# Kernel optimization log

Hardware: AMD Instinct MI355X
Metric: run time of the kernel (lower is better)

The kernel has to match this reference:

```python
import jax, jax.numpy as jnp
import numpy as np

B, TV, TS, DIN, D = 32, 1024, 64, 1024, 512
EPS = 1e-15


def setup_inputs() -> dict:
    key = jax.random.key(0)
    k1, k2, k3, k4, k5, k6 = jax.random.split(key, 6)
    videos = jax.random.normal(k1, (B, TV, DIN), dtype=jnp.float32)
    sentences = jax.random.normal(k2, (B, TS, DIN), dtype=jnp.float32)
    lengths = jax.random.randint(k3, (B,), 1, TS, dtype=jnp.int32)
    scale = 1.0 / np.sqrt(DIN)
    Wv = jax.random.normal(k4, (DIN, D), dtype=jnp.float32) * scale
    bv = jnp.zeros((D,), dtype=jnp.float32)
    Ws = jax.random.normal(k5, (DIN, D), dtype=jnp.float32) * scale
    bs = jnp.zeros((D,), dtype=jnp.float32)
    return {"videos": videos, "sentences": sentences, "lengths": lengths,
            "Wv": Wv, "bv": bv, "Ws": Ws, "bs": bs}


def _pair_score(V, S):
    # V: [TV, D] video repr for item i; S: [TS, D] sentence repr for item j
    nv = jnp.linalg.norm(V, axis=1)                      # [TV]
    ns = jnp.linalg.norm(S, axis=1)                      # [TS]
    # cosine-similarity coattention matrix via normalized matmul (no repeat/tile)
    C = (V @ S.T) / (nv[:, None] * ns[None, :] + EPS)    # [TV, TS]
    A = jax.nn.softmax(C, axis=1)                        # normalize over sentence axis
    att = A @ S                                          # [TV, D] sentence attention
    num = jnp.sum(V * att, axis=1)                       # [TV]
    den = nv * jnp.linalg.norm(att, axis=1)
    score = num / (den + EPS)                            # [TV] per-frame video score
    return jax.nn.logsumexp(score)                       # scalar


def reference(videos, sentences, lengths, Wv, bv, Ws, bs):
    # per-timestep dense encoders (video_layer / sentence_layer)
    videos_repr = jnp.einsum('btf,fd->btd', videos, Wv) + bv      # [B, TV, D]
    sentences_repr = jnp.einsum('bsf,fd->bsd', sentences, Ws) + bs  # [B, TS, D]
    # all-pairs (i video, j sentence) scores, vectorized over the B x B grid
    pairwise = jax.vmap(lambda V: jax.vmap(lambda S: _pair_score(V, S))(sentences_repr))
    scores_videos = pairwise(videos_repr)                # [B, B]
    return scores_videos
```

## Files before the change

### kernel.cpp

```cpp
#include <hip/hip_runtime.h>
#include <hip/hip_bf16.h>
#include <stdint.h>
#include <math.h>

typedef __attribute__((ext_vector_type(8))) __bf16 bf16x8;
typedef __attribute__((ext_vector_type(4))) float f32x4;

#define B_   32
#define TV_  1024
#define TS_  64
#define DIN_ 1024
#define D_   512

static __device__ __forceinline__ unsigned short f2bf(float f) {
    union { float f; uint32_t u; } x; x.f = f;
    uint32_t r = x.u + 0x7fffu + ((x.u >> 16) & 1u);
    return (unsigned short)(r >> 16);
}
static __device__ __forceinline__ uint32_t cvtpk(float lo, float hi) {
    uint32_t r;
    asm("v_cvt_pk_bf16_f32 %0, %1, %2" : "=v"(r) : "v"(lo), "v"(hi));
    return r;
}
static __device__ __forceinline__ void swap32(uint32_t& a, uint32_t& b) {
    asm volatile("v_permlane32_swap_b32 %0, %1" : "+v"(a), "+v"(b));
}
static __device__ __forceinline__ void swap16(uint32_t& a, uint32_t& b) {
    asm volatile("v_permlane16_swap_b32 %0, %1" : "+v"(a), "+v"(b));
}
static __device__ __forceinline__ void gload16(const void* g, void* l) {
    __builtin_amdgcn_global_load_lds((const __attribute__((address_space(1))) uint32_t*)g,
                                     (__attribute__((address_space(3))) uint32_t*)l, 16, 0, 0);
}

__global__ __launch_bounds__(256) void transpose_w(const float* __restrict__ Wv,
                                                   const float* __restrict__ Wsn,
                                                   unsigned short* __restrict__ Wt) {
    const int w = blockIdx.z;
    const float* src = w ? Wsn : Wv;
    __shared__ float t[32][33];
    const int k0 = blockIdx.x * 32, n0 = blockIdx.y * 32;
    const int tx = threadIdx.x & 31, ty = threadIdx.x >> 5;
    #pragma unroll
    for (int r = 0; r < 32; r += 8)
        t[r + ty][tx] = src[(size_t)(k0 + r + ty) * D_ + n0 + tx];
    __syncthreads();
    #pragma unroll
    for (int r = 0; r < 32; r += 8)
        Wt[(size_t)w * 524288 + (size_t)(n0 + r + ty) * DIN_ + k0 + tx] = f2bf(t[tx][r + ty]);
}

__global__ __launch_bounds__(256) void encoder_gemm(const float* __restrict__ videos,
                                                    const float* __restrict__ sentences,
                                                    const unsigned short* __restrict__ Wt,
                                                    const float* __restrict__ bv,
                                                    const float* __restrict__ bs,
                                                    unsigned short* __restrict__ Vrep,
                                                    unsigned short* __restrict__ Srep) {
    __shared__ char Asb[128 * 128];
    __shared__ char Bsb[128 * 128];
    const int bid = blockIdx.x;
    const float* X; const unsigned short* W; const float* bias; unsigned short* out;
    int m0, n0;
    if (bid < 1024) {
        int xcd = bid & 7, sl = bid >> 3;
        m0 = (xcd * 32 + (sl >> 2)) * 128;
        n0 = (sl & 3) * 128;
        X = videos; W = Wt; bias = bv; out = Vrep;
    } else {
        int sb = bid - 1024;
        m0 = (sb >> 2) * 128;
        n0 = (sb & 3) * 128;
        X = sentences; W = Wt + 524288; bias = bs; out = Srep;
    }
    const int tid = threadIdx.x;
    const int lane = tid & 63, wid = tid >> 6;
    const int g = lane >> 4, c = lane & 15;
    const int wm = wid >> 1, wn = wid & 1;

    f32x4 acc[4][4];
    {
        f32x4 z = {0.f, 0.f, 0.f, 0.f};
        #pragma unroll
        for (int a = 0; a < 4; ++a)
            #pragma unroll
            for (int b = 0; b < 4; ++b) acc[a][b] = z;
    }

    for (int kk = 0; kk < 16; ++kk) {
        const int k0 = kk * 64;
        #pragma unroll
        for (int it = 0; it < 8; ++it) {
            int idx = it * 256 + tid;
            int m = idx >> 4, k4 = idx & 15;
            float4 v = *(const float4*)(X + (size_t)(m0 + m) * DIN_ + k0 + k4 * 4);
            uint2 pk;
            pk.x = cvtpk(v.x, v.y);
            pk.y = cvtpk(v.z, v.w);
            *(uint2*)(Asb + m * 128 + ((k4 * 8) ^ ((m & 7) << 4))) = pk;
        }
        #pragma unroll
        for (int t = 0; t < 4; ++t) {
            int row = wid * 32 + t * 8 + (lane >> 3);
            const unsigned short* src = W + (size_t)(n0 + row) * DIN_ + k0 + (lane & 7) * 8;
            gload16(src, Bsb + wid * 4096 + t * 1024);
        }
        __syncthreads();
        #pragma unroll
        for (int ks = 0; ks < 2; ++ks) {
            bf16x8 a[4], b[4];
            #pragma unroll
            for (int mt = 0; mt < 4; ++mt) {
                int row = wm * 64 + mt * 16 + c;
                a[mt] = *(const bf16x8*)(Asb + row * 128 + ((g * 16 + ks * 64) ^ ((c & 7) << 4)));
            }
            #pragma unroll
            for (int nt = 0; nt < 4; ++nt) {
                int rowb = wn * 64 + nt * 16 + c;
                b[nt] = *(const bf16x8*)(Bsb + rowb * 128 + (g * 16 + ks * 64));
            }
            #pragma unroll
            for (int mt = 0; mt < 4; ++mt)
                #pragma unroll
                for (int nt = 0; nt < 4; ++nt)
                    acc[mt][nt] = __builtin_amdgcn_mfma_f32_16x16x32_bf16(a[mt], b[nt], acc[mt][nt], 0, 0, 0);
        }
        __syncthreads();
    }
    #pragma unroll
    for (int nt = 0; nt < 4; ++nt) {
        int col = n0 + wn * 64 + nt * 16 + c;
        float bb = bias[col];
        #pragma unroll
        for (int mt = 0; mt < 4; ++mt) {
            int rbase = m0 + wm * 64 + mt * 16 + g * 4;
            #pragma unroll
            for (int r = 0; r < 4; ++r)
                out[(size_t)(rbase + r) * D_ + col] = f2bf(acc[mt][nt][r] + bb);
        }
    }
}

__global__ __launch_bounds__(256) void rownorm_kernel(const unsigned short* __restrict__ R,
                                                      float* __restrict__ nrm, int nrows) {
    const int row = blockIdx.x * 4 + (threadIdx.x >> 6);
    const int lane = threadIdx.x & 63;
    if (row >= nrows) return;
    uint4 v = ((const uint4*)(R + (size_t)row * D_))[lane];
    float s = 0.f;
    uint32_t wsx[4] = {v.x, v.y, v.z, v.w};
    #pragma unroll
    for (int q = 0; q < 4; ++q) {
        float lo = __uint_as_float(wsx[q] << 16);
        float hi = __uint_as_float(wsx[q] & 0xffff0000u);
        s += lo * lo + hi * hi;
    }
    #pragma unroll
    for (int d = 1; d < 64; d <<= 1) s += __shfl_xor(s, d);
    if (lane == 0) nrm[row] = sqrtf(s);
}

__global__ __launch_bounds__(256) void gram_kernel(const unsigned short* __restrict__ S,
                                                   unsigned short* __restrict__ Gn,
                                                   unsigned short* __restrict__ Sf,
                                                   float* __restrict__ lgns) {
    const int i = blockIdx.x;
    const int tid = threadIdx.x, lane = tid & 63, w = tid >> 6;
    const int g = lane >> 4, c = lane & 15;
    const unsigned short* Sp = S + (size_t)i * TS_ * D_;
    __shared__ float rns_sh[64];

    {
        const int row = tid >> 2, q = tid & 3;
        const uint4* rp = (const uint4*)(Sp + (size_t)row * D_ + q * 128);
        float s = 0.f;
        #pragma unroll
        for (int e = 0; e < 16; ++e) {
            uint4 v = rp[e];
            uint32_t wsx[4] = {v.x, v.y, v.z, v.w};
            #pragma unroll
            for (int qq = 0; qq < 4; ++qq) {
                float lo = __uint_as_float(wsx[qq] << 16);
                float hi = __uint_as_float(wsx[qq] & 0xffff0000u);
                s += lo * lo + hi * hi;
            }
        }
        s += __shfl_xor(s, 1);
        s += __shfl_xor(s, 2);
        if (q == 0) {
            rns_sh[row] = rsqrtf(s);
            lgns[i * 64 + row] = 0.5f * log2f(s);
        }
    }
    __syncthreads();

    {
        f32x4 acc[4];
        {
            f32x4 z = {0.f, 0.f, 0.f, 0.f};
            #pragma unroll
            for (int a = 0; a < 4; ++a) acc[a] = z;
        }
        #pragma unroll
        for (int ks = 0; ks < 16; ++ks) {
            bf16x8 a = *(const bf16x8*)(Sp + (size_t)(w * 16 + c) * D_ + ks * 32 + g * 8);
            #pragma unroll
            for (int nt = 0; nt < 4; ++nt) {
                bf16x8 b = *(const bf16x8*)(Sp + (size_t)(nt * 16 + c) * D_ + ks * 32 + g * 8);
                acc[nt] = __builtin_amdgcn_mfma_f32_16x16x32_bf16(a, b, acc[nt], 0, 0, 0);
            }
        }
        #pragma unroll
        for (int nt = 0; nt < 4; ++nt)
            #pragma unroll
            for (int r = 0; r < 4; ++r) {
                int R = w * 16 + g * 4 + r, C = nt * 16 + c;
                float vn = acc[nt][r] * rns_sh[R] * rns_sh[C];
                int idx = (w * 2 + (nt >> 1)) * 512 + (((nt & 1) * 2 + (c >> 3)) * 16 + g * 4 + r) * 8 + (c & 7);
                Gn[(size_t)i * 4096 + idx] = f2bf(vn);
            }
    }

    #pragma unroll
    for (int t = 0; t < 16; ++t) {
        int idx = t * 256 + tid;
        int ks = idx >> 8, at = (idx >> 6) & 3, ln = idx & 63;
        int row = at * 16 + (ln & 15), gg = ln >> 4;
        uint4 raw = *(const uint4*)(Sp + (size_t)row * D_ + ks * 32 + gg * 8);
        float sc = rns_sh[row];
        uint32_t rw[4] = {raw.x, raw.y, raw.z, raw.w};
        uint4 o;
        uint32_t* op = (uint32_t*)&o;
        #pragma unroll
        for (int q = 0; q < 4; ++q) {
            float lo = __uint_as_float(rw[q] << 16) * sc;
            float hi = __uint_as_float(rw[q] & 0xffff0000u) * sc;
            op[q] = cvtpk(lo, hi);
        }
        *(uint4*)(Sf + (size_t)i * 32768 + idx * 8) = o;
    }
}

__global__ __launch_bounds__(512, 2) void pairwise_kernel(const unsigned short* __restrict__ V,
                                                          const unsigned short* __restrict__ Sf,
                                                          const unsigned short* __restrict__ Gn,
                                                          const float* __restrict__ nv,
                                                          const float* __restrict__ lgns,
                                                          float* __restrict__ outp) {
    __shared__ char Ssh[131072];
    __shared__ char Gsh[16384];
    __shared__ float lgsh[128];
    __shared__ float wsum[16];

    const int bid = blockIdx.x;
    const int xcd = bid & 7, slot = bid >> 3;
    const int i = xcd + 8 * (slot >> 4);
    const int jp = slot & 15;
    const int tid = threadIdx.x;
    const int lane = tid & 63, w = tid >> 6;
    const int g = lane >> 4, c = lane & 15;
    const float L2E = 1.4426950408889634f;

    {
        const unsigned short* Sjf = Sf + (size_t)jp * 65536;
        #pragma unroll
        for (int it = 0; it < 16; ++it) {
            int idx = it * 512 + tid;
            *(uint4*)(Ssh + idx * 16) = *(const uint4*)(Sjf + idx * 8);
        }
        const unsigned short* Gp = Gn + (size_t)jp * 8192;
        #pragma unroll
        for (int it = 0; it < 2; ++it) {
            int idx = it * 512 + tid;
            *(uint4*)(Gsh + idx * 16) = *(const uint4*)(Gp + idx * 8);
        }
        if (tid < 32) *(float4*)(lgsh + tid * 4) = *(const float4*)(lgns + jp * 128 + tid * 4);
    }
    __syncthreads();

    const unsigned short* Vb[2];
    #pragma unroll
    for (int mt = 0; mt < 2; ++mt)
        Vb[mt] = V + ((size_t)i * TV_ + w * 32 + mt * 16 + c) * D_ + g * 8;
    const float* nvb = nv + i * TV_ + w * 32 + c;

    float s_run0 = 0.0f, s_run1 = 0.0f;

    for (int chunk = 0; chunk < 4; ++chunk) {
        const size_t coff = (size_t)chunk * 256 * D_;
        f32x4 acc[2][8];
        {
            f32x4 z = {0.f, 0.f, 0.f, 0.f};
            #pragma unroll
            for (int a = 0; a < 2; ++a)
                #pragma unroll
                for (int b = 0; b < 8; ++b) acc[a][b] = z;
        }
        bf16x8 bcur[2], bnxt[2];
        #pragma unroll
        for (int mt = 0; mt < 2; ++mt) bcur[mt] = *(const bf16x8*)(Vb[mt] + coff);
        #pragma unroll
        for (int ks = 0; ks < 16; ++ks) {
            bf16x8 a[8];
            #pragma unroll
            for (int q = 0; q < 8; ++q)
                a[q] = *(const bf16x8*)(Ssh + ((q >> 2) << 16) + (((ks * 4 + (q & 3))) << 10) + lane * 16);
            if (ks < 15) {
                #pragma unroll
                for (int mt = 0; mt < 2; ++mt)
                    bnxt[mt] = *(const bf16x8*)(Vb[mt] + coff + (ks + 1) * 32);
            }
            __builtin_amdgcn_s_setprio(1);
            #pragma unroll
            for (int mt = 0; mt < 2; ++mt)
                #pragma unroll
                for (int q = 0; q < 8; ++q)
                    acc[mt][q] = __builtin_amdgcn_mfma_f32_16x16x32_bf16(a[q], bcur[mt], acc[mt][q], 0, 0, 0);
            __builtin_amdgcn_s_setprio(0);
            #pragma unroll
            for (int mt = 0; mt < 2; ++mt) bcur[mt] = bnxt[mt];
        }

        float nv4[2], rnv[2];
        #pragma unroll
        for (int mt = 0; mt < 2; ++mt) {
            nv4[mt] = nvb[chunk * 256 + mt * 16];
            rnv[mt] = __builtin_amdgcn_rcpf(nv4[mt]);
        }

        #pragma unroll
        for (int jj = 0; jj < 2; ++jj) {
            float lg[16];
            #pragma unroll
            for (int at = 0; at < 4; ++at) {
                float4 t4 = *(const float4*)(lgsh + jj * 64 + at * 16 + g * 4);
                lg[at * 4 + 0] = t4.x; lg[at * 4 + 1] = t4.y;
                lg[at * 4 + 2] = t4.z; lg[at * 4 + 3] = t4.w;
            }
            float SPC[2], SPQ[2] = {0.f, 0.f};
            uint32_t bfr[2][2][4];
            #pragma unroll
            for (int mt = 0; mt < 2; ++mt) {
                float rnvL = rnv[mt] * L2E;
                float SPCm = 0.f;
                #pragma unroll
                for (int at = 0; at < 4; ++at)
                    #pragma unroll
                    for (int r = 0; r < 4; ++r) {
                        float t = acc[mt][jj * 4 + at][r];
                        float e = exp2f(fmaf(t, rnvL, lg[at * 4 + r]));
                        SPCm = fmaf(e, t, SPCm);
                        acc[mt][jj * 4 + at][r] = e;
                    }
                SPC[mt] = SPCm;
                #pragma unroll
                for (int ks2 = 0; ks2 < 2; ++ks2) {
                    const int a0 = jj * 4 + ks2 * 2, a1 = a0 + 1;
                    uint32_t A  = cvtpk(acc[mt][a0][0], acc[mt][a0][1]);
                    uint32_t Bw = cvtpk(acc[mt][a0][2], acc[mt][a0][3]);
                    uint32_t C  = cvtpk(acc[mt][a1][0], acc[mt][a1][1]);
                    uint32_t Dw = cvtpk(acc[mt][a1][2], acc[mt][a1][3]);
                    swap32(A, C);  swap16(A, C);
                    swap32(Bw, Dw); swap16(Bw, Dw);
                    bfr[mt][ks2][0] = A;  bfr[mt][ks2][1] = Bw;
                    bfr[mt][ks2][2] = C;  bfr[mt][ks2][3] = Dw;
                }
            }
            #pragma unroll
            for (int st = 0; st < 4; ++st) {
                bf16x8 g0 = *(const bf16x8*)(Gsh + (jj << 13) + ((st * 2 + 0) << 10) + lane * 16);
                bf16x8 g1 = *(const bf16x8*)(Gsh + (jj << 13) + ((st * 2 + 1) << 10) + lane * 16);
                __builtin_amdgcn_s_setprio(1);
                #pragma unroll
                for (int mt = 0; mt < 2; ++mt) {
                    union { uint32_t u[4]; bf16x8 v; } f0, f1;
                    #pragma unroll
                    for (int q = 0; q < 4; ++q) { f0.u[q] = bfr[mt][0][q]; f1.u[q] = bfr[mt][1][q]; }
                    f32x4 d2 = {0.f, 0.f, 0.f, 0.f};
                    d2 = __builtin_amdgcn_mfma_f32_16x16x32_bf16(g0, f0.v, d2, 0, 0, 0);
                    d2 = __builtin_amdgcn_mfma_f32_16x16x32_bf16(g1, f1.v, d2, 0, 0, 0);
                    #pragma unroll
                    for (int r = 0; r < 4; ++r) SPQ[mt] += acc[mt][jj * 4 + st][r] * d2[r];
                }
                __builtin_amdgcn_s_setprio(0);
            }

            #pragma unroll
            for (int mt = 0; mt < 2; ++mt) {
                float SPCm = SPC[mt], SPQm = SPQ[mt];
                SPCm += __shfl_xor(SPCm, 16); SPCm += __shfl_xor(SPCm, 32);
                SPQm += __shfl_xor(SPQm, 16); SPQm += __shfl_xor(SPQm, 32);
                float sc = SPCm * rnv[mt] * rsqrtf(fmaxf(SPQm, 1e-20f));
                float ev = exp2f(sc * L2E);
                if (jj == 0) s_run0 += ev; else s_run1 += ev;
            }
        }
    }

    #pragma unroll
    for (int d = 1; d < 16; d <<= 1) {
        s_run0 += __shfl_xor(s_run0, d);
        s_run1 += __shfl_xor(s_run1, d);
    }
    if (lane == 0) { wsum[w * 2] = s_run0; wsum[w * 2 + 1] = s_run1; }
    __syncthreads();
    if (tid < 2) {
        float total = 0.f;
        #pragma unroll
        for (int ww = 0; ww < 8; ++ww) total += wsum[ww * 2 + tid];
        outp[i * 32 + jp * 2 + tid] = 0.69314718055994531f * log2f(total);
    }
}

extern "C" void kernel_launch(void* const* d_in, const int* in_sizes, int n_in,
                              void* d_out, int out_size, void* d_ws, size_t ws_size,
                              hipStream_t stream) {
    const float* videos    = (const float*)d_in[0];
    const float* sentences = (const float*)d_in[1];
    const float* Wv  = (const float*)d_in[3];
    const float* bv  = (const float*)d_in[4];
    const float* Wsn = (const float*)d_in[5];
    const float* bs  = (const float*)d_in[6];
    float* outp = (float*)d_out;

    char* ws = (char*)d_ws;
    unsigned short* Vrep = (unsigned short*)(ws);
    unsigned short* Srep = (unsigned short*)(ws + 33554432);
    unsigned short* Wt   = (unsigned short*)(ws + 35651584);
    unsigned short* Gn   = (unsigned short*)(ws + 37748736);
    float*          nv   = (float*)(ws + 38010880);
    float*          lgns = (float*)(ws + 38141952);
    unsigned short* Sf   = Wt;

    transpose_w<<<dim3(32, 16, 2), 256, 0, stream>>>(Wv, Wsn, Wt);
    encoder_gemm<<<1088, 256, 0, stream>>>(videos, sentences, Wt, bv, bs, Vrep, Srep);
    rownorm_kernel<<<8192, 256, 0, stream>>>(Vrep, nv, B_ * TV_);
    gram_kernel<<<B_, 256, 0, stream>>>(Srep, Gn, Sf, lgns);
    pairwise_kernel<<<512, 512, 0, stream>>>(Vrep, Sf, Gn, nv, lgns, outp);
}
```

Before: 189.2 us.

## Double-buffer encoder GEMM tiles with register prefetch and swizzled B layout

The encoder GEMM now prefetches the next K tile into registers while MFMAs run on the current LDS buffer, then writes it into a second LDS buffer. This lets global-load latency overlap compute and needs only one barrier per iteration. The B tile moves from direct global-to-LDS loads to register loads with an XOR-swizzled layout to cut bank conflicts, and MFMA sections get raised wave priority. In exchange LDS use doubles to 64KB per block and register pressure rises, which may lower occupancy.

```diff
diff --git a/kernel.cpp b/kernel.cpp
--- a/kernel.cpp
+++ b/kernel.cpp
@@ -27,10 +27,6 @@
 }
 static __device__ __forceinline__ void swap16(uint32_t& a, uint32_t& b) {
     asm volatile("v_permlane16_swap_b32 %0, %1" : "+v"(a), "+v"(b));
-}
-static __device__ __forceinline__ void gload16(const void* g, void* l) {
-    __builtin_amdgcn_global_load_lds((const __attribute__((address_space(1))) uint32_t*)g,
-                                     (__attribute__((address_space(3))) uint32_t*)l, 16, 0, 0);
 }
 
 __global__ __launch_bounds__(256) void transpose_w(const float* __restrict__ Wv,
@@ -57,8 +53,8 @@
                                                     const float* __restrict__ bs,
                                                     unsigned short* __restrict__ Vrep,
                                                     unsigned short* __restrict__ Srep) {
-    __shared__ char Asb[128 * 128];
-    __shared__ char Bsb[128 * 128];
+    __shared__ char Asb[2][16384];
+    __shared__ char Bsb[2][16384];
     const int bid = blockIdx.x;
     const float* X; const unsigned short* W; const float* bias; unsigned short* out;
     int m0, n0;
@@ -78,6 +74,13 @@
     const int g = lane >> 4, c = lane & 15;
     const int wm = wid >> 1, wn = wid & 1;
 
+    const int am = tid >> 4, ak4 = tid & 15;
+    const int bn = tid >> 3, bkq = tid & 7;
+    const float* Ag = X + (size_t)(m0 + am) * DIN_ + ak4 * 4;
+    const unsigned short* Bg = W + (size_t)(n0 + bn) * DIN_ + bkq * 8;
+    char* Aw0 = &Asb[0][am * 128 + ((ak4 * 8) ^ ((am & 7) << 4))];
+    char* Bw0 = &Bsb[0][bn * 128 + ((bkq * 16) ^ ((bn & 7) << 4))];
+
     f32x4 acc[4][4];
     {
         f32x4 z = {0.f, 0.f, 0.f, 0.f};
@@ -87,46 +90,66 @@
             for (int b = 0; b < 4; ++b) acc[a][b] = z;
     }
 
+    float4 av[8]; uint4 bvv[4];
+    #define LOADTILE(kk) {                                                     \
+        const int k0_ = (kk) * 64;                                             \
+        _Pragma("unroll")                                                      \
+        for (int it = 0; it < 8; ++it)                                         \
+            av[it] = *(const float4*)(Ag + (size_t)(it * 16) * DIN_ + k0_);    \
+        _Pragma("unroll")                                                      \
+        for (int it = 0; it < 4; ++it)                                         \
+            bvv[it] = *(const uint4*)(Bg + (size_t)(it * 32) * DIN_ + k0_);    \
+    }
+    #define WRITETILE(buf) {                                                   \
+        _Pragma("unroll")                                                      \
+        for (int it = 0; it < 8; ++it) {                                       \
+            uint2 pk;                                                          \
+            pk.x = cvtpk(av[it].x, av[it].y);                                  \
+            pk.y = cvtpk(av[it].z, av[it].w);                                  \
+            *(uint2*)(Aw0 + (buf) * 16384 + it * 2048) = pk;                   \
+        }                                                                      \
+        _Pragma("unroll")                                                      \
+        for (int it = 0; it < 4; ++it)                                         \
+            *(uint4*)(Bw0 + (buf) * 16384 + it * 4096) = bvv[it];              \
+    }
+
+    LOADTILE(0);
+    WRITETILE(0);
+    __syncthreads();
+    int cur = 0;
+
     for (int kk = 0; kk < 16; ++kk) {
-        const int k0 = kk * 64;
-        #pragma unroll
-        for (int it = 0; it < 8; ++it) {
-            int idx = it * 256 + tid;
-            int m = idx >> 4, k4 = idx & 15;
-            float4 v = *(const float4*)(X + (size_t)(m0 + m) * DIN_ + k0 + k4 * 4);
-            uint2 pk;
-            pk.x = cvtpk(v.x, v.y);
-            pk.y = cvtpk(v.z, v.w);
-            *(uint2*)(Asb + m * 128 + ((k4 * 8) ^ ((m & 7) << 4))) = pk;
-        }
-        #pragma unroll
-        for (int t = 0; t < 4; ++t) {
-            int row = wid * 32 + t * 8 + (lane >> 3);
-            const unsigned short* src = W + (size_t)(n0 + row) * DIN_ + k0 + (lane & 7) * 8;
-            gload16(src, Bsb + wid * 4096 + t * 1024);
-        }
-        __syncthreads();
+        if (kk < 15) LOADTILE(kk + 1);
         #pragma unroll
         for (int ks = 0; ks < 2; ++ks) {
             bf16x8 a[4], b[4];
             #pragma unroll
             for (int mt = 0; mt < 4; ++mt) {
                 int row = wm * 64 + mt * 16 + c;
-                a[mt] = *(const bf16x8*)(Asb + row * 128 + ((g * 16 + ks * 64) ^ ((c & 7) << 4)));
+                a[mt] = *(const bf16x8*)(&Asb[cur][0] + row * 128 + ((g * 16 + ks * 64) ^ ((c & 7) << 4)));
             }
             #pragma unroll
             for (int nt = 0; nt < 4; ++nt) {
                 int rowb = wn * 64 + nt * 16 + c;
-                b[nt] = *(const bf16x8*)(Bsb + rowb * 128 + (g * 16 + ks * 64));
-            }
+                b[nt] = *(const bf16x8*)(&Bsb[cur][0] + rowb * 128 + ((g * 16 + ks * 64) ^ ((c & 7) << 4)));
+            }
+            __builtin_amdgcn_s_setprio(1);
             #pragma unroll
             for (int mt = 0; mt < 4; ++mt)
                 #pragma unroll
                 for (int nt = 0; nt < 4; ++nt)
                     acc[mt][nt] = __builtin_amdgcn_mfma_f32_16x16x32_bf16(a[mt], b[nt], acc[mt][nt], 0, 0, 0);
-        }
-        __syncthreads();
-    }
+            __builtin_amdgcn_s_setprio(0);
+        }
+        if (kk < 15) {
+            WRITETILE(cur ^ 1);
+            __syncthreads();
+            cur ^= 1;
+        }
+    }
+    #undef LOADTILE
+    #undef WRITETILE
+
     #pragma unroll
     for (int nt = 0; nt < 4; ++nt) {
         int col = n0 + wn * 64 + nt * 16 + c;
```

After: 209.1 us. 1.11x slower.
